# Optimization experiments

Measured on AMD Instinct MI355X. Metric: run time of the kernel, lower is better.

Reference implementation:

```python
import jax, jax.numpy as jnp
import numpy as np

NUM_EMBEDDING = 512
EMBEDDING_DIM = 64
COMMITMENT_COST = 0.25


def setup_inputs() -> dict:
    key = jax.random.key(0)
    k1, k2 = jax.random.split(key)
    inputs = jax.random.normal(k1, (32, EMBEDDING_DIM, 64, 64), dtype=jnp.float32)
    # nn.Embedding weight init: uniform(-1/K, 1/K)
    weight = jax.random.uniform(
        k2, (NUM_EMBEDDING, EMBEDDING_DIM), dtype=jnp.float32,
        minval=-1.0 / NUM_EMBEDDING, maxval=1.0 / NUM_EMBEDDING)
    return {"inputs": inputs, "weight": weight}


def reference(inputs, weight):
    B, C, H, W = inputs.shape  # C == EMBEDDING_DIM
    K = weight.shape[0]
    sg = jax.lax.stop_gradient

    # NCHW -> NHWC -> [N, D]
    x = jnp.transpose(inputs, (0, 2, 3, 1)).reshape(-1, C)

    distances = (jnp.sum(x * x, axis=1, keepdims=True)
                 + jnp.sum(weight * weight, axis=1)
                 - 2.0 * jnp.matmul(x, weight.T))
    encoding_indices = jnp.argmin(distances, axis=1)  # [N]

    # one-hot scatter, as in the original
    encodings = jax.nn.one_hot(encoding_indices, K, dtype=x.dtype)  # [N, K]
    # quantized = encodings @ E  (== gather E[idx])
    quantized = jnp.matmul(encodings, weight)  # [N, D]

    q_latent_loss = jnp.mean((sg(quantized) - x) ** 2)
    e_latent_loss = jnp.mean((quantized - sg(x)) ** 2)
    loss = q_latent_loss + COMMITMENT_COST * e_latent_loss

    # straight-through estimator
    quantized_st = x + sg(quantized - x)

    avg_probs = jnp.mean(encodings, axis=0)  # [K]
    perplexity = jnp.exp(-jnp.sum(avg_probs * jnp.log(avg_probs + 1e-10)))

    # [N, D] -> [B, H, W, D] -> [B, D, H, W]
    quantized_out = jnp.transpose(quantized_st.reshape(B, H, W, C), (0, 3, 1, 2))
    return loss, quantized_out, perplexity, encodings
```

## Files before the change

kernel.cpp:

```cpp
#include <hip/hip_runtime.h>

#define BHW 262144
#define OUT_Q_OFF 1
#define OUT_P_OFF 8388609
#define OUT_E_OFF 8388610

#define IDX_W 17664

typedef __attribute__((ext_vector_type(8))) short short8;
typedef __attribute__((ext_vector_type(4))) float f32x4;
typedef __attribute__((ext_vector_type(2))) float f32x2;

__device__ __forceinline__ unsigned short f2bf(float f) {
    union { float f; unsigned u; } c; c.f = f;
    unsigned r = (c.u + 0x7FFFu + ((c.u >> 16) & 1u)) >> 16;
    return (unsigned short)r;
}

__global__ __launch_bounds__(512) void vq_init(const float* __restrict__ W, float* __restrict__ ws) {
    const int tid = blockIdx.x * 512 + threadIdx.x;
    if (tid < 512) {
        const float4* W4 = (const float4*)W;
        float s = 0.f;
#pragma unroll
        for (int i = 0; i < 16; ++i) {
            float4 v = W4[tid * 16 + i];
            s = fmaf(v.x, v.x, s); s = fmaf(v.y, v.y, s);
            s = fmaf(v.z, v.z, s); s = fmaf(v.w, v.w, s);
        }
        ws[768 + tid] = s;
    } else {
        const int c  = tid - 512;
        const int l  = c & 63;
        const int j  = (c >> 6) & 1;
        const int tn = c >> 7;
        const int n  = tn * 16 + (l & 15);
        const int k0 = j * 32 + ((l >> 4) & 3) * 8;
        const float* src = W + n * 64 + k0;
        unsigned h0 = f2bf(-2.f * src[0]) | ((unsigned)f2bf(-2.f * src[1]) << 16);
        unsigned h1 = f2bf(-2.f * src[2]) | ((unsigned)f2bf(-2.f * src[3]) << 16);
        unsigned h2 = f2bf(-2.f * src[4]) | ((unsigned)f2bf(-2.f * src[5]) << 16);
        unsigned h3 = f2bf(-2.f * src[6]) | ((unsigned)f2bf(-2.f * src[7]) << 16);
        uint4* dst = (uint4*)(ws + 1280);
        dst[c] = make_uint4(h0, h1, h2, h3);
    }
}

__global__ __launch_bounds__(256) void vq_main(const float* __restrict__ X,
                                               const float* __restrict__ W,
                                               float* __restrict__ out,
                                               float* __restrict__ ws) {
    const int t    = threadIdx.x;
    const int l    = t & 63;
    const int wv   = t >> 6;
    const int nlow = l & 15;
    const int kg   = l >> 4;
    const int rowbase = blockIdx.x * 64;
    const int b = rowbase >> 12;
    const int h = (rowbase >> 6) & 63;
    const int myrow = wv * 16 + nlow;

    __shared__ short8 Btab[2048];

    const float* xr = X + (size_t)b * BHW + (size_t)h * 64 + myrow;
    float xf[16];
#pragma unroll
    for (int e = 0; e < 8; ++e) xf[e]     = xr[(size_t)(kg * 8 + e) * 4096];
#pragma unroll
    for (int e = 0; e < 8; ++e) xf[8 + e] = xr[(size_t)(32 + kg * 8 + e) * 4096];
    short8 a0, a1;
#pragma unroll
    for (int e = 0; e < 8; ++e) { a0[e] = (short)f2bf(xf[e]); a1[e] = (short)f2bf(xf[8 + e]); }

    const uint4* __restrict__ gtab = (const uint4*)(ws + 1280);
    const float* __restrict__ wsq  = ws + 768;
    float bS[4]; int bK[4];
#pragma unroll
    for (int r = 0; r < 4; ++r) { bS[r] = 3.4e38f; bK[r] = 0; }

    for (int half = 0; half < 2; ++half) {
        __syncthreads();
        uint4* bt = (uint4*)Btab;
#pragma unroll
        for (int i = 0; i < 8; ++i)
            bt[i * 256 + t] = gtab[half * 2048 + i * 256 + t];
        __syncthreads();
#pragma unroll 4
        for (int tn = 0; tn < 16; ++tn) {
            short8 f0 = Btab[tn * 128 + l];
            short8 f1 = Btab[tn * 128 + 64 + l];
            const int   n  = (half * 16 + tn) * 16 + nlow;
            const float wq = wsq[n];
            f32x4 acc = {wq, wq, wq, wq};
            acc = __builtin_amdgcn_mfma_f32_16x16x32_bf16(a0, f0, acc, 0, 0, 0);
            acc = __builtin_amdgcn_mfma_f32_16x16x32_bf16(a1, f1, acc, 0, 0, 0);
#pragma unroll
            for (int r = 0; r < 4; ++r) {
                if (acc[r] < bS[r]) { bS[r] = acc[r]; bK[r] = n; }
            }
        }
    }
#pragma unroll
    for (int r = 0; r < 4; ++r) {
#pragma unroll
        for (int mask = 1; mask <= 8; mask <<= 1) {
            float os = __shfl_xor(bS[r], mask);
            int   ok = __shfl_xor(bK[r], mask);
            if (os < bS[r] || (os == bS[r] && ok < bK[r])) { bS[r] = os; bK[r] = ok; }
        }
    }

    int rowBk = 0;
    int myBk  = 0;
    f32x2* encB = (f32x2*)(out + OUT_E_OFF);
    const size_t Rbase = (size_t)(rowbase + wv * 16);
#pragma unroll
    for (int m = 0; m < 16; ++m) {
        int bkm = __shfl(bK[m & 3], (m >> 2) * 16);
        if (nlow == m) rowBk = bkm;
        if (l == m)    myBk = bkm;
        f32x2* erow = encB + (Rbase + m) * 256;
#pragma unroll
        for (int c = 0; c < 4; ++c) {
            int p = c * 64 + l;
            f32x2 v;
            v.x = (bkm == 2 * p)     ? 1.f : 0.f;
            v.y = (bkm == 2 * p + 1) ? 1.f : 0.f;
            erow[p] = v;
        }
    }
    if (l < 16) ((int*)ws)[IDX_W + rowbase + wv * 16 + l] = myBk;

    const float4* W4 = (const float4*)W;
    float4 q0 = W4[rowBk * 16 + kg * 2];
    float4 q1 = W4[rowBk * 16 + kg * 2 + 1];
    float4 q2 = W4[rowBk * 16 + 8 + kg * 2];
    float4 q3 = W4[rowBk * 16 + 8 + kg * 2 + 1];
    float qv[16] = {q0.x, q0.y, q0.z, q0.w, q1.x, q1.y, q1.z, q1.w,
                    q2.x, q2.y, q2.z, q2.w, q3.x, q3.y, q3.z, q3.w};
    float lsum = 0.f;
    float* op = out + OUT_Q_OFF + (size_t)b * BHW + (size_t)h * 64 + myrow;
#pragma unroll
    for (int e = 0; e < 8; ++e) {
        float d0 = qv[e] - xf[e];
        lsum = fmaf(d0, d0, lsum);
        op[(size_t)(kg * 8 + e) * 4096] = xf[e] + d0;
        float d1 = qv[8 + e] - xf[8 + e];
        lsum = fmaf(d1, d1, lsum);
        op[(size_t)(32 + kg * 8 + e) * 4096] = xf[8 + e] + d1;
    }

#pragma unroll
    for (int off = 32; off >= 1; off >>= 1) lsum += __shfl_down(lsum, off);
    if (l == 0) atomicAdd(ws + ((blockIdx.x * 4 + wv) & 255), lsum);
}

__global__ __launch_bounds__(512) void vq_fin(const float* __restrict__ ws, float* __restrict__ out) {
    __shared__ unsigned hist[512];
    __shared__ float redP[8], redL[8];
    const int t = threadIdx.x;
    hist[t] = 0u;
    __syncthreads();
    const uint4* __restrict__ idx4 = (const uint4*)((const int*)ws + IDX_W);
#pragma unroll 4
    for (int i = 0; i < 64; ++i) {
        uint4 v = idx4[i * 512 + t];
        atomicAdd(&hist[v.x], 1u);
        atomicAdd(&hist[v.y], 1u);
        atomicAdd(&hist[v.z], 1u);
        atomicAdd(&hist[v.w], 1u);
    }
    __syncthreads();
    float p = (float)hist[t] * (1.0f / 131072.0f);
    float s = p * logf(p + 1e-10f);
    float lp = (t < 256) ? ws[t] : 0.f;
#pragma unroll
    for (int off = 32; off >= 1; off >>= 1) {
        s  += __shfl_down(s, off);
        lp += __shfl_down(lp, off);
    }
    if ((t & 63) == 0) { redP[t >> 6] = s; redL[t >> 6] = lp; }
    __syncthreads();
    if (t == 0) {
        float tp = 0.f, tl = 0.f;
#pragma unroll
        for (int i = 0; i < 8; ++i) { tp += redP[i]; tl += redL[i]; }
        out[OUT_P_OFF] = expf(-tp);
        out[0] = tl * (1.25f / 8388608.0f);
    }
}

extern "C" void kernel_launch(void* const* d_in, const int* in_sizes, int n_in,
                              void* d_out, int out_size, void* d_ws, size_t ws_size,
                              hipStream_t stream) {
    const float* X = (const float*)d_in[0];
    const float* W = (const float*)d_in[1];
    float* out = (float*)d_out;
    float* ws  = (float*)d_ws;

    (void)hipMemsetAsync(d_ws, 0, 256 * sizeof(float), stream);
    vq_init<<<9, 512, 0, stream>>>(W, ws);
    vq_main<<<2048, 256, 0, stream>>>(X, W, out, ws);
    vq_fin<<<1, 512, 0, stream>>>(ws, out);
}
```

Measured before the change: 112.7 us.

## Stage input/output tiles through LDS for vectorized access; read codebook from global

Each block now loads its 64x64 NCHW input tile with coalesced float4 loads into a padded shared-memory transpose buffer, and each lane reads its 16 channels from there. The straight-through output goes back through the same buffer and is written with 16-byte vector stores. The bf16 codebook table is no longer copied into LDS in two halves with barriers; waves read it directly from global memory and rely on L1/L2 caching. This cuts strided scalar global traffic but adds extra cache pressure on the codebook. The float4 output stores sit at a one-float offset, so they are not 16-byte aligned.

Measured after the change: 112.3 us. Within noise of the previous version (-0.3%).

```diff
diff --git a/kernel.cpp b/kernel.cpp
--- a/kernel.cpp
+++ b/kernel.cpp
@@ -60,44 +60,48 @@
     const int h = (rowbase >> 6) & 63;
     const int myrow = wv * 16 + nlow;
 
-    __shared__ short8 Btab[2048];
-
-    const float* xr = X + (size_t)b * BHW + (size_t)h * 64 + myrow;
+    __shared__ float xt[64 * 65];
+
+    const float4* __restrict__ X4 = (const float4*)X;
+    const int base4 = b * 65536 + h * 16;
+#pragma unroll
+    for (int i = 0; i < 4; ++i) {
+        int flat = i * 256 + t;
+        int c  = flat >> 4;
+        int w4 = flat & 15;
+        float4 v = X4[base4 + c * 1024 + w4];
+        int o = c * 65 + w4 * 4;
+        xt[o] = v.x; xt[o + 1] = v.y; xt[o + 2] = v.z; xt[o + 3] = v.w;
+    }
+    __syncthreads();
+
     float xf[16];
 #pragma unroll
-    for (int e = 0; e < 8; ++e) xf[e]     = xr[(size_t)(kg * 8 + e) * 4096];
-#pragma unroll
-    for (int e = 0; e < 8; ++e) xf[8 + e] = xr[(size_t)(32 + kg * 8 + e) * 4096];
+    for (int e = 0; e < 8; ++e) xf[e]     = xt[(kg * 8 + e) * 65 + myrow];
+#pragma unroll
+    for (int e = 0; e < 8; ++e) xf[8 + e] = xt[(32 + kg * 8 + e) * 65 + myrow];
     short8 a0, a1;
 #pragma unroll
     for (int e = 0; e < 8; ++e) { a0[e] = (short)f2bf(xf[e]); a1[e] = (short)f2bf(xf[8 + e]); }
 
-    const uint4* __restrict__ gtab = (const uint4*)(ws + 1280);
-    const float* __restrict__ wsq  = ws + 768;
+    const short8* __restrict__ B8  = (const short8*)(ws + 1280);
+    const float*  __restrict__ wsq = ws + 768;
     float bS[4]; int bK[4];
 #pragma unroll
     for (int r = 0; r < 4; ++r) { bS[r] = 3.4e38f; bK[r] = 0; }
 
-    for (int half = 0; half < 2; ++half) {
-        __syncthreads();
-        uint4* bt = (uint4*)Btab;
-#pragma unroll
-        for (int i = 0; i < 8; ++i)
-            bt[i * 256 + t] = gtab[half * 2048 + i * 256 + t];
-        __syncthreads();
-#pragma unroll 4
-        for (int tn = 0; tn < 16; ++tn) {
-            short8 f0 = Btab[tn * 128 + l];
-            short8 f1 = Btab[tn * 128 + 64 + l];
-            const int   n  = (half * 16 + tn) * 16 + nlow;
-            const float wq = wsq[n];
-            f32x4 acc = {wq, wq, wq, wq};
-            acc = __builtin_amdgcn_mfma_f32_16x16x32_bf16(a0, f0, acc, 0, 0, 0);
-            acc = __builtin_amdgcn_mfma_f32_16x16x32_bf16(a1, f1, acc, 0, 0, 0);
-#pragma unroll
-            for (int r = 0; r < 4; ++r) {
-                if (acc[r] < bS[r]) { bS[r] = acc[r]; bK[r] = n; }
-            }
+#pragma unroll 2
+    for (int tn = 0; tn < 32; ++tn) {
+        short8 f0 = B8[tn * 128 + l];
+        short8 f1 = B8[tn * 128 + 64 + l];
+        const float wq = wsq[tn * 16 + nlow];
+        f32x4 acc = {wq, wq, wq, wq};
+        acc = __builtin_amdgcn_mfma_f32_16x16x32_bf16(a0, f0, acc, 0, 0, 0);
+        acc = __builtin_amdgcn_mfma_f32_16x16x32_bf16(a1, f1, acc, 0, 0, 0);
+        const int n = tn * 16 + nlow;
+#pragma unroll
+        for (int r = 0; r < 4; ++r) {
+            if (acc[r] < bS[r]) { bS[r] = acc[r]; bK[r] = n; }
         }
     }
 #pragma unroll
@@ -138,21 +142,36 @@
     float4 q3 = W4[rowBk * 16 + 8 + kg * 2 + 1];
     float qv[16] = {q0.x, q0.y, q0.z, q0.w, q1.x, q1.y, q1.z, q1.w,
                     q2.x, q2.y, q2.z, q2.w, q3.x, q3.y, q3.z, q3.w};
+    float st[16];
     float lsum = 0.f;
-    float* op = out + OUT_Q_OFF + (size_t)b * BHW + (size_t)h * 64 + myrow;
-#pragma unroll
-    for (int e = 0; e < 8; ++e) {
-        float d0 = qv[e] - xf[e];
-        lsum = fmaf(d0, d0, lsum);
-        op[(size_t)(kg * 8 + e) * 4096] = xf[e] + d0;
-        float d1 = qv[8 + e] - xf[8 + e];
-        lsum = fmaf(d1, d1, lsum);
-        op[(size_t)(32 + kg * 8 + e) * 4096] = xf[8 + e] + d1;
-    }
+#pragma unroll
+    for (int e = 0; e < 16; ++e) {
+        float d = qv[e] - xf[e];
+        lsum = fmaf(d, d, lsum);
+        st[e] = xf[e] + d;
+    }
+    __syncthreads();
+#pragma unroll
+    for (int e = 0; e < 8; ++e) xt[(kg * 8 + e) * 65 + myrow]      = st[e];
+#pragma unroll
+    for (int e = 0; e < 8; ++e) xt[(32 + kg * 8 + e) * 65 + myrow] = st[8 + e];
 
 #pragma unroll
     for (int off = 32; off >= 1; off >>= 1) lsum += __shfl_down(lsum, off);
     if (l == 0) atomicAdd(ws + ((blockIdx.x * 4 + wv) & 255), lsum);
+    __syncthreads();
+
+    float4* __restrict__ O4 = (float4*)(out + OUT_Q_OFF);
+#pragma unroll
+    for (int i = 0; i < 4; ++i) {
+        int flat = i * 256 + t;
+        int c  = flat >> 4;
+        int w4 = flat & 15;
+        int o = c * 65 + w4 * 4;
+        f32x4 v = {xt[o], xt[o + 1], xt[o + 2], xt[o + 3]};
+        f32x4* dst = (f32x4*)(out + OUT_Q_OFF + (size_t)b * BHW + (size_t)c * 4096 + h * 64 + w4 * 4);
+        *dst = v;
+    }
 }
 
 __global__ __launch_bounds__(512) void vq_fin(const float* __restrict__ ws, float* __restrict__ out) {
```

## Process 32 rows per wave and read codebook fragments directly from global

Applied to the files above, without the earlier changes.

Each wavefront now handles two 16-row tiles and reuses every loaded codebook fragment for two MFMA chains. The LDS staging of the codebook table and its block barriers are dropped, and fragments are read straight from the L2-resident workspace. The grid is halved to keep total coverage. This raises per-thread register use and relies on cache hits for the B fragments instead of shared memory.

Result: slower. 118.6 us (+5.2%).

```diff
diff --git a/kernel.cpp b/kernel.cpp
--- a/kernel.cpp
+++ b/kernel.cpp
@@ -55,99 +55,125 @@
     const int wv   = t >> 6;
     const int nlow = l & 15;
     const int kg   = l >> 4;
-    const int rowbase = blockIdx.x * 64;
-    const int b = rowbase >> 12;
-    const int h = (rowbase >> 6) & 63;
-    const int myrow = wv * 16 + nlow;
-
-    __shared__ short8 Btab[2048];
-
-    const float* xr = X + (size_t)b * BHW + (size_t)h * 64 + myrow;
-    float xf[16];
-#pragma unroll
-    for (int e = 0; e < 8; ++e) xf[e]     = xr[(size_t)(kg * 8 + e) * 4096];
-#pragma unroll
-    for (int e = 0; e < 8; ++e) xf[8 + e] = xr[(size_t)(32 + kg * 8 + e) * 4096];
-    short8 a0, a1;
-#pragma unroll
-    for (int e = 0; e < 8; ++e) { a0[e] = (short)f2bf(xf[e]); a1[e] = (short)f2bf(xf[8 + e]); }
-
-    const uint4* __restrict__ gtab = (const uint4*)(ws + 1280);
-    const float* __restrict__ wsq  = ws + 768;
-    float bS[4]; int bK[4];
-#pragma unroll
-    for (int r = 0; r < 4; ++r) { bS[r] = 3.4e38f; bK[r] = 0; }
-
-    for (int half = 0; half < 2; ++half) {
-        __syncthreads();
-        uint4* bt = (uint4*)Btab;
-#pragma unroll
-        for (int i = 0; i < 8; ++i)
-            bt[i * 256 + t] = gtab[half * 2048 + i * 256 + t];
-        __syncthreads();
+    const int rowbase = (blockIdx.x * 4 + wv) * 32;
+    const int b  = rowbase >> 12;
+    const int h  = (rowbase >> 6) & 63;
+    const int w0 = rowbase & 63;
+
+    const float* xr0 = X + (size_t)b * BHW + (size_t)h * 64 + (w0 + nlow);
+    const float* xr1 = xr0 + 16;
+    float xf0[16], xf1[16];
+#pragma unroll
+    for (int e = 0; e < 8; ++e) {
+        xf0[e]     = xr0[(size_t)(kg * 8 + e) * 4096];
+        xf0[8 + e] = xr0[(size_t)(32 + kg * 8 + e) * 4096];
+        xf1[e]     = xr1[(size_t)(kg * 8 + e) * 4096];
+        xf1[8 + e] = xr1[(size_t)(32 + kg * 8 + e) * 4096];
+    }
+    short8 a00, a01, a10, a11;
+#pragma unroll
+    for (int e = 0; e < 8; ++e) {
+        a00[e] = (short)f2bf(xf0[e]); a01[e] = (short)f2bf(xf0[8 + e]);
+        a10[e] = (short)f2bf(xf1[e]); a11[e] = (short)f2bf(xf1[8 + e]);
+    }
+
+    const short8* __restrict__ B8  = (const short8*)(ws + 1280);
+    const float*  __restrict__ wsq = ws + 768;
+    float bS0[4], bS1[4]; int bK0[4], bK1[4];
+#pragma unroll
+    for (int r = 0; r < 4; ++r) { bS0[r] = 3.4e38f; bK0[r] = 0; bS1[r] = 3.4e38f; bK1[r] = 0; }
+
 #pragma unroll 4
-        for (int tn = 0; tn < 16; ++tn) {
-            short8 f0 = Btab[tn * 128 + l];
-            short8 f1 = Btab[tn * 128 + 64 + l];
-            const int   n  = (half * 16 + tn) * 16 + nlow;
-            const float wq = wsq[n];
-            f32x4 acc = {wq, wq, wq, wq};
-            acc = __builtin_amdgcn_mfma_f32_16x16x32_bf16(a0, f0, acc, 0, 0, 0);
-            acc = __builtin_amdgcn_mfma_f32_16x16x32_bf16(a1, f1, acc, 0, 0, 0);
-#pragma unroll
-            for (int r = 0; r < 4; ++r) {
-                if (acc[r] < bS[r]) { bS[r] = acc[r]; bK[r] = n; }
-            }
+    for (int tn = 0; tn < 32; ++tn) {
+        short8 f0 = B8[tn * 128 + l];
+        short8 f1 = B8[tn * 128 + 64 + l];
+        const float wq = wsq[tn * 16 + nlow];
+        const int   n  = tn * 16 + nlow;
+        f32x4 acc0 = {wq, wq, wq, wq};
+        f32x4 acc1 = {wq, wq, wq, wq};
+        acc0 = __builtin_amdgcn_mfma_f32_16x16x32_bf16(a00, f0, acc0, 0, 0, 0);
+        acc1 = __builtin_amdgcn_mfma_f32_16x16x32_bf16(a10, f0, acc1, 0, 0, 0);
+        acc0 = __builtin_amdgcn_mfma_f32_16x16x32_bf16(a01, f1, acc0, 0, 0, 0);
+        acc1 = __builtin_amdgcn_mfma_f32_16x16x32_bf16(a11, f1, acc1, 0, 0, 0);
+#pragma unroll
+        for (int r = 0; r < 4; ++r) {
+            if (acc0[r] < bS0[r]) { bS0[r] = acc0[r]; bK0[r] = n; }
+            if (acc1[r] < bS1[r]) { bS1[r] = acc1[r]; bK1[r] = n; }
         }
     }
 #pragma unroll
     for (int r = 0; r < 4; ++r) {
 #pragma unroll
         for (int mask = 1; mask <= 8; mask <<= 1) {
-            float os = __shfl_xor(bS[r], mask);
-            int   ok = __shfl_xor(bK[r], mask);
-            if (os < bS[r] || (os == bS[r] && ok < bK[r])) { bS[r] = os; bK[r] = ok; }
-        }
-    }
-
-    int rowBk = 0;
-    int myBk  = 0;
+            float os; int ok;
+            os = __shfl_xor(bS0[r], mask); ok = __shfl_xor(bK0[r], mask);
+            if (os < bS0[r] || (os == bS0[r] && ok < bK0[r])) { bS0[r] = os; bK0[r] = ok; }
+            os = __shfl_xor(bS1[r], mask); ok = __shfl_xor(bK1[r], mask);
+            if (os < bS1[r] || (os == bS1[r] && ok < bK1[r])) { bS1[r] = os; bK1[r] = ok; }
+        }
+    }
+
+    const int src = (nlow >> 2) * 16;
+    int g0, g1, g2, g3, sel = nlow & 3;
+    g0 = __shfl(bK0[0], src); g1 = __shfl(bK0[1], src);
+    g2 = __shfl(bK0[2], src); g3 = __shfl(bK0[3], src);
+    const int rowBk0 = sel == 0 ? g0 : sel == 1 ? g1 : sel == 2 ? g2 : g3;
+    g0 = __shfl(bK1[0], src); g1 = __shfl(bK1[1], src);
+    g2 = __shfl(bK1[2], src); g3 = __shfl(bK1[3], src);
+    const int rowBk1 = sel == 0 ? g0 : sel == 1 ? g1 : sel == 2 ? g2 : g3;
+
+    if (l < 32) ((int*)ws)[IDX_W + rowbase + l] = (l < 16) ? rowBk0 : rowBk1;
+
+    const float4* W4 = (const float4*)W;
+    float4 p0 = W4[rowBk0 * 16 + kg * 2];
+    float4 p1 = W4[rowBk0 * 16 + kg * 2 + 1];
+    float4 p2 = W4[rowBk0 * 16 + 8 + kg * 2];
+    float4 p3 = W4[rowBk0 * 16 + 8 + kg * 2 + 1];
+    float4 s0 = W4[rowBk1 * 16 + kg * 2];
+    float4 s1 = W4[rowBk1 * 16 + kg * 2 + 1];
+    float4 s2 = W4[rowBk1 * 16 + 8 + kg * 2];
+    float4 s3 = W4[rowBk1 * 16 + 8 + kg * 2 + 1];
+
     f32x2* encB = (f32x2*)(out + OUT_E_OFF);
-    const size_t Rbase = (size_t)(rowbase + wv * 16);
+    const size_t R0 = (size_t)rowbase;
+    const size_t R1 = (size_t)rowbase + 16;
 #pragma unroll
     for (int m = 0; m < 16; ++m) {
-        int bkm = __shfl(bK[m & 3], (m >> 2) * 16);
-        if (nlow == m) rowBk = bkm;
-        if (l == m)    myBk = bkm;
-        f32x2* erow = encB + (Rbase + m) * 256;
+        const int bkm0 = __shfl(bK0[m & 3], (m >> 2) * 16);
+        const int bkm1 = __shfl(bK1[m & 3], (m >> 2) * 16);
+        f32x2* e0 = encB + (R0 + m) * 256;
+        f32x2* e1 = encB + (R1 + m) * 256;
 #pragma unroll
         for (int c = 0; c < 4; ++c) {
-            int p = c * 64 + l;
-            f32x2 v;
-            v.x = (bkm == 2 * p)     ? 1.f : 0.f;
-            v.y = (bkm == 2 * p + 1) ? 1.f : 0.f;
-            erow[p] = v;
-        }
-    }
-    if (l < 16) ((int*)ws)[IDX_W + rowbase + wv * 16 + l] = myBk;
-
-    const float4* W4 = (const float4*)W;
-    float4 q0 = W4[rowBk * 16 + kg * 2];
-    float4 q1 = W4[rowBk * 16 + kg * 2 + 1];
-    float4 q2 = W4[rowBk * 16 + 8 + kg * 2];
-    float4 q3 = W4[rowBk * 16 + 8 + kg * 2 + 1];
-    float qv[16] = {q0.x, q0.y, q0.z, q0.w, q1.x, q1.y, q1.z, q1.w,
-                    q2.x, q2.y, q2.z, q2.w, q3.x, q3.y, q3.z, q3.w};
+            const int p = c * 64 + l;
+            f32x2 v0, v1;
+            v0.x = (bkm0 == 2 * p)     ? 1.f : 0.f;
+            v0.y = (bkm0 == 2 * p + 1) ? 1.f : 0.f;
+            v1.x = (bkm1 == 2 * p)     ? 1.f : 0.f;
+            v1.y = (bkm1 == 2 * p + 1) ? 1.f : 0.f;
+            e0[p] = v0;
+            e1[p] = v1;
+        }
+    }
+
+    float qa[16] = {p0.x, p0.y, p0.z, p0.w, p1.x, p1.y, p1.z, p1.w,
+                    p2.x, p2.y, p2.z, p2.w, p3.x, p3.y, p3.z, p3.w};
+    float qb[16] = {s0.x, s0.y, s0.z, s0.w, s1.x, s1.y, s1.z, s1.w,
+                    s2.x, s2.y, s2.z, s2.w, s3.x, s3.y, s3.z, s3.w};
     float lsum = 0.f;
-    float* op = out + OUT_Q_OFF + (size_t)b * BHW + (size_t)h * 64 + myrow;
+    float* op0 = out + OUT_Q_OFF + (size_t)b * BHW + (size_t)h * 64 + (w0 + nlow);
+    float* op1 = op0 + 16;
 #pragma unroll
     for (int e = 0; e < 8; ++e) {
-        float d0 = qv[e] - xf[e];
-        lsum = fmaf(d0, d0, lsum);
-        op[(size_t)(kg * 8 + e) * 4096] = xf[e] + d0;
-        float d1 = qv[8 + e] - xf[8 + e];
-        lsum = fmaf(d1, d1, lsum);
-        op[(size_t)(32 + kg * 8 + e) * 4096] = xf[8 + e] + d1;
+        float d;
+        d = qa[e] - xf0[e];          lsum = fmaf(d, d, lsum);
+        op0[(size_t)(kg * 8 + e) * 4096] = xf0[e] + d;
+        d = qa[8 + e] - xf0[8 + e];  lsum = fmaf(d, d, lsum);
+        op0[(size_t)(32 + kg * 8 + e) * 4096] = xf0[8 + e] + d;
+        d = qb[e] - xf1[e];          lsum = fmaf(d, d, lsum);
+        op1[(size_t)(kg * 8 + e) * 4096] = xf1[e] + d;
+        d = qb[8 + e] - xf1[8 + e];  lsum = fmaf(d, d, lsum);
+        op1[(size_t)(32 + kg * 8 + e) * 4096] = xf1[8 + e] + d;
     }
 
 #pragma unroll
@@ -200,6 +226,6 @@
 
     (void)hipMemsetAsync(d_ws, 0, 256 * sizeof(float), stream);
     vq_init<<<9, 512, 0, stream>>>(W, ws);
-    vq_main<<<2048, 256, 0, stream>>>(X, W, out, ws);
+    vq_main<<<1024, 256, 0, stream>>>(X, W, out, ws);
     vq_fin<<<1, 512, 0, stream>>>(ws, out);
 }
```
